# Optimization experiments

Hardware: AMD Instinct MI355X
Metric: run time of the kernel (lower is better)

## Reference

```python
import jax, jax.numpy as jnp
import numpy as np

ALPHA = 0.2  # LeakyReLU negative slope
NEG_INF = -9e15


def _xavier(key, shape, gain=1.414):
    fan_in, fan_out = shape[-2], shape[-1]
    lim = gain * np.sqrt(6.0 / (fan_in + fan_out))
    return jax.random.uniform(key, shape, jnp.float32, -lim, lim)


def setup_inputs() -> dict:
    key = jax.random.key(0)
    ks = jax.random.split(key, 8)
    B, N, Din, H, Dh, Do = 8, 1024, 256, 4, 128, 64
    x = jax.random.normal(ks[0], (B, N, Din), jnp.float32)
    adj = jax.random.randint(ks[1], (B, N, N), 0, 2).astype(jnp.int32)
    W_heads = _xavier(ks[2], (H, Din, Dh))                 # per-head W
    a_heads = _xavier(ks[3], (H, 2 * Dh, 1))[..., 0]       # per-head a, [H, 2*Dh]
    W_out = _xavier(ks[4], (H * Dh, Do))                   # out_att W
    a_out = _xavier(ks[5], (2 * Do, 1))[..., 0]            # out_att a, [2*Do]
    Wf = _xavier(ks[6], (Do, Do), gain=1.0)                # fc_out linear
    bf = jnp.zeros((Do,), jnp.float32)
    return {"x": x, "adj": adj, "W_heads": W_heads, "a_heads": a_heads,
            "W_out": W_out, "a_out": a_out, "Wf": Wf, "bf": bf}


def _leaky_relu(v):
    return jnp.where(v >= 0, v, ALPHA * v)


def _gat(h, adj, W, a):
    # h: [B,N,Fin], adj: [B,N,N], W: [Fin,Fout], a: [2*Fout]
    Wh = h @ W                                   # [B,N,F]
    F = W.shape[-1]
    # additive attention: e_ij = leakyrelu(a_src.Wh_i + a_dst.Wh_j)
    src = Wh @ a[:F]                             # [B,N]
    dst = Wh @ a[F:]                             # [B,N]
    e = _leaky_relu(src[:, :, None] + dst[:, None, :])   # [B,N,N]
    scores = jnp.where(adj > 0, e, NEG_INF)
    attn = jax.nn.softmax(scores, axis=-1)       # dropout is a no-op in eval
    return attn @ Wh                             # [B,N,F]


def reference(x, adj, W_heads, a_heads, W_out, a_out, Wf, bf):
    B, N, _ = x.shape
    H, _, Dh = W_heads.shape
    # multi-head GAT, heads vmapped over leading axis of W_heads / a_heads
    heads = jax.vmap(_gat, in_axes=(None, None, 0, 0))(x, adj, W_heads, a_heads)  # [H,B,N,Dh]
    xcat = jnp.moveaxis(heads, 0, 2).reshape(B, N, H * Dh)   # concat heads, dim=2
    out = jax.nn.elu(_gat(xcat, adj, W_out, a_out))           # [B,N,Do]
    out = jax.nn.relu(out @ Wf + bf)                          # fc_out (dropout no-op)
    return out
```

## Files before the change

### kernel.cpp

```cpp
#include <hip/hip_runtime.h>
#include <hip/hip_bf16.h>

#define BSZ 8
#define NN 1024
#define DIN 256
#define NH 4
#define DH 128
#define DOUT 64
#define RTOT (BSZ*NN)
#define FCAT (NH*DH)
#define ALPHA 0.2f
#define XBLK 1024

typedef unsigned short ushortT;
typedef __attribute__((ext_vector_type(8))) short bf16x8;
typedef __attribute__((ext_vector_type(4))) float f32x4;

static __device__ __forceinline__ ushortT f2bf(float f) {
    __hip_bfloat16 h = __float2bfloat16(f);
    return *reinterpret_cast<ushortT*>(&h);
}
static __device__ __forceinline__ float bfu2f(ushortT u) {
    return __uint_as_float(((unsigned)u) << 16);
}
static __device__ __forceinline__ void split2(float v, ushortT& hi, ushortT& lo) {
    hi = f2bf(v);
    lo = f2bf(v - bfu2f(hi));
}
static __device__ __forceinline__ void gload16(const ushortT* g, ushortT* l) {
    __builtin_amdgcn_global_load_lds(
        (const __attribute__((address_space(1))) unsigned int*)(const void*)g,
        (__attribute__((address_space(3))) unsigned int*)(void*)l, 16, 0, 0);
}

__global__ __launch_bounds__(256) void k_prepw(const float* __restrict__ x,
                                               const float* __restrict__ W,
                                               const float* __restrict__ Wout,
                                               ushortT* __restrict__ xbh, ushortT* __restrict__ xbl,
                                               ushortT* __restrict__ WbTh, ushortT* __restrict__ WbTl,
                                               ushortT* __restrict__ WoTh, ushortT* __restrict__ WoTl) {
    const int bx = blockIdx.x;
    if (bx < XBLK) {
        const int g = bx * 256 + threadIdx.x;
        const float4* p = (const float4*)x + (size_t)g * 2;
        union { ushortT u[8]; uint4 q; } th, tl;
#pragma unroll
        for (int e4 = 0; e4 < 2; ++e4) {
            const float4 v = p[e4];
            split2(v.x, th.u[e4 * 4 + 0], tl.u[e4 * 4 + 0]);
            split2(v.y, th.u[e4 * 4 + 1], tl.u[e4 * 4 + 1]);
            split2(v.z, th.u[e4 * 4 + 2], tl.u[e4 * 4 + 2]);
            split2(v.w, th.u[e4 * 4 + 3], tl.u[e4 * 4 + 3]);
        }
        ((uint4*)xbh)[g] = th.q;
        ((uint4*)xbl)[g] = tl.q;
        return;
    }
    const int g2 = (bx - XBLK) * 256 + threadIdx.x;
    if (g2 < NH * DH * DIN) {
        const int h = g2 >> 15, f = (g2 >> 8) & 127, k = g2 & 255;
        const int kt = k >> 6, k64 = k & 63;
        const float v = W[(size_t)h * DIN * DH + (size_t)k * DH + f];
        ushortT hi, lo; split2(v, hi, lo);
        const int idx = ((h * 4 + kt) * 128 + f) * 64 + k64;
        WbTh[idx] = hi; WbTl[idx] = lo;
    } else {
        const int g3 = g2 - NH * DH * DIN;
        const int f = g3 >> 9, k = g3 & 511;
        const float v = Wout[(size_t)k * DOUT + f];
        ushortT hi, lo; split2(v, hi, lo);
        WoTh[g3] = hi; WoTl[g3] = lo;
    }
}

__global__ __launch_bounds__(512) void k_main(const ushortT* __restrict__ xbh,
                                              const ushortT* __restrict__ xbl,
                                              const float* __restrict__ ah_,
                                              const ushortT* __restrict__ WbTh,
                                              const ushortT* __restrict__ WbTl,
                                              const int* __restrict__ adj,
                                              unsigned* __restrict__ adjbit,
                                              ushortT* __restrict__ WhT,
                                              float* __restrict__ src1,
                                              float* __restrict__ dst1) {
    __shared__ ushortT Ah[128 * 64], Al[128 * 64];
    __shared__ ushortT Bh[128 * 64], Bl[128 * 64];
    __shared__ float sred[8][32], dred[8][32];
    const int tid = threadIdx.x;
    if (blockIdx.x >= 256) {
        const int g = (blockIdx.x - 256) * 512 + tid;
        const int row = g >> 5, w = g & 31;
        const int4* p = (const int4*)(adj + (size_t)row * NN + w * 32);
        unsigned m = 0;
#pragma unroll
        for (int q = 0; q < 8; ++q) {
            const int4 v = p[q];
            m |= (v.x > 0 ? 1u : 0u) << (q * 4 + 0);
            m |= (v.y > 0 ? 1u : 0u) << (q * 4 + 1);
            m |= (v.z > 0 ? 1u : 0u) << (q * 4 + 2);
            m |= (v.w > 0 ? 1u : 0u) << (q * 4 + 3);
        }
        adjbit[g] = m;
        return;
    }
    const int lane = tid & 63, wave = tid >> 6;
    const int h = blockIdx.x >> 6, mt = blockIdx.x & 63;
    const int r0 = mt * 128, b = r0 >> 10, jr = r0 & 1023;
    const int m16 = lane & 15, quad = lane >> 4;
    const int mg = wave >> 1, fg = wave & 1;
    f32x4 acc[2][4];
#pragma unroll
    for (int a = 0; a < 2; ++a)
#pragma unroll
        for (int c = 0; c < 4; ++c) acc[a][c] = (f32x4){0.f, 0.f, 0.f, 0.f};

    for (int kt = 0; kt < 4; ++kt) {
        __syncthreads();
        const ushortT* planeH = WbTh + (size_t)((h * 4 + kt) * 128) * 64;
        const ushortT* planeL = WbTl + (size_t)((h * 4 + kt) * 128) * 64;
#pragma unroll
        for (int half = 0; half < 2; ++half) {
            const int f = wave * 16 + half * 8 + (lane >> 3);
            const int sc = (lane & 7) ^ (f & 7);
            gload16(planeH + (size_t)f * 64 + sc * 8, Bh + (wave * 16 + half * 8) * 64);
            gload16(planeL + (size_t)f * 64 + sc * 8, Bl + (wave * 16 + half * 8) * 64);
        }
#pragma unroll
        for (int half = 0; half < 2; ++half) {
            const int r = wave * 16 + half * 8 + (lane >> 3);
            const int sc = (lane & 7) ^ (r & 7);
            gload16(xbh + (size_t)(r0 + r) * DIN + kt * 64 + sc * 8, Ah + (wave * 16 + half * 8) * 64);
            gload16(xbl + (size_t)(r0 + r) * DIN + kt * 64 + sc * 8, Al + (wave * 16 + half * 8) * 64);
        }
        __syncthreads();
#pragma unroll
        for (int ks = 0; ks < 2; ++ks) {
            bf16x8 a_h[2], a_l[2], b_h[4], b_l[4];
#pragma unroll
            for (int ms = 0; ms < 2; ++ms) {
                const int row = (mg * 2 + ms) * 16 + m16;
                const int cl = (ks * 4 + quad) ^ (row & 7);
                a_h[ms] = *(const bf16x8*)&Ah[row * 64 + cl * 8];
                a_l[ms] = *(const bf16x8*)&Al[row * 64 + cl * 8];
            }
#pragma unroll
            for (int fs = 0; fs < 4; ++fs) {
                const int row = (fg * 4 + fs) * 16 + m16;
                const int cl = (ks * 4 + quad) ^ (row & 7);
                b_h[fs] = *(const bf16x8*)&Bh[row * 64 + cl * 8];
                b_l[fs] = *(const bf16x8*)&Bl[row * 64 + cl * 8];
            }
#pragma unroll
            for (int ms = 0; ms < 2; ++ms)
#pragma unroll
                for (int fs = 0; fs < 4; ++fs) {
                    acc[ms][fs] = __builtin_amdgcn_mfma_f32_16x16x32_bf16(a_h[ms], b_h[fs], acc[ms][fs], 0, 0, 0);
                    acc[ms][fs] = __builtin_amdgcn_mfma_f32_16x16x32_bf16(a_h[ms], b_l[fs], acc[ms][fs], 0, 0, 0);
                    acc[ms][fs] = __builtin_amdgcn_mfma_f32_16x16x32_bf16(a_l[ms], b_h[fs], acc[ms][fs], 0, 0, 0);
                }
        }
    }
    float sacc[2][4] = {{0,0,0,0},{0,0,0,0}}, dacc[2][4] = {{0,0,0,0},{0,0,0,0}};
#pragma unroll
    for (int ms = 0; ms < 2; ++ms)
#pragma unroll
        for (int fs = 0; fs < 4; ++fs) {
            const int fl = (fg * 4 + fs) * 16 + m16;
            const float a_s = ah_[h * 2 * DH + fl];
            const float a_d = ah_[h * 2 * DH + DH + fl];
            union { ushortT u[4]; uint2 q; } tw;
#pragma unroll
            for (int reg = 0; reg < 4; ++reg) {
                const float v = acc[ms][fs][reg];
                sacc[ms][reg] += v * a_s;
                dacc[ms][reg] += v * a_d;
                tw.u[reg] = f2bf(v);
            }
            *(uint2*)(WhT + ((size_t)((b * NH + h) * DH + fl)) * NN + jr + (mg * 2 + ms) * 16 + quad * 4) = tw.q;
        }
#pragma unroll
    for (int ms = 0; ms < 2; ++ms) {
#pragma unroll
        for (int reg = 0; reg < 4; ++reg) {
            float s = sacc[ms][reg], d = dacc[ms][reg];
#pragma unroll
            for (int o = 8; o > 0; o >>= 1) {
                s += __shfl_xor(s, o, 64);
                d += __shfl_xor(d, o, 64);
            }
            if (m16 == 0) {
                sred[wave][ms * 16 + quad * 4 + reg] = s;
                dred[wave][ms * 16 + quad * 4 + reg] = d;
            }
        }
    }
    __syncthreads();
    if (tid < 128) {
        const int mgr = tid >> 5, idx = tid & 31;
        src1[h * RTOT + r0 + tid] = sred[mgr * 2][idx] + sred[mgr * 2 + 1][idx];
        dst1[h * RTOT + r0 + tid] = dred[mgr * 2][idx] + dred[mgr * 2 + 1][idx];
    }
}

__global__ __launch_bounds__(512) void k_attn1(const unsigned* __restrict__ adjbit,
                                               const ushortT* __restrict__ WhT,
                                               const float* __restrict__ src1,
                                               const float* __restrict__ dst1,
                                               ushortT* __restrict__ xcat) {
    __shared__ ushortT As[2][64 * 64];
    __shared__ ushortT Bs[2][128 * 64];
    __shared__ unsigned maskS[64 * 32];
    __shared__ float dstv[NN];
    __shared__ float srcv[64], rowinv[64], red8[8];
    const int tid = threadIdx.x, lane = tid & 63, wave = tid >> 6;
    const int bh = blockIdx.x & 31, it = blockIdx.x >> 5;
    const int b = bh >> 2, h = bh & 3;
    const int i0 = it * 64;
    const int m16 = lane & 15, quad = lane >> 4;
    const int mg = wave >> 2, fg = wave & 3;

    const unsigned* mbase = adjbit + (size_t)(b * NN + i0) * 32;
#pragma unroll
    for (int k2 = 0; k2 < 4; ++k2) maskS[tid + 512 * k2] = mbase[tid + 512 * k2];
    float lm = -INFINITY;
#pragma unroll
    for (int k2 = 0; k2 < 2; ++k2) {
        const float d = dst1[h * RTOT + b * NN + tid + 512 * k2];
        dstv[tid + 512 * k2] = d;
        lm = fmaxf(lm, d);
    }
    if (tid < 64) srcv[tid] = src1[h * RTOT + b * NN + i0 + tid];
#pragma unroll
    for (int o = 32; o > 0; o >>= 1) lm = fmaxf(lm, __shfl_xor(lm, o, 64));
    if (lane == 0) red8[wave] = lm;
    __syncthreads();
    float dmax = red8[0];
#pragma unroll
    for (int w = 1; w < 8; ++w) dmax = fmaxf(dmax, red8[w]);

    const int arow = tid >> 3, apart = tid & 7;
    const float si = srcv[arow];
    float mrow = si + dmax;
    mrow = mrow >= 0.f ? mrow : ALPHA * mrow;
    float fsum = 0.f;

    const ushortT* Bbase = WhT + (size_t)(bh * DH) * NN;
    f32x4 acc[2][2];
#pragma unroll
    for (int a = 0; a < 2; ++a)
#pragma unroll
        for (int c = 0; c < 2; ++c) acc[a][c] = (f32x4){0.f, 0.f, 0.f, 0.f};

#define STAGE_TILE(kt_, buf_)                                                              \
    {                                                                                      \
        const int kt__ = (kt_);                                                            \
        ushortT* bdst = &Bs[(buf_)][0];                                                    \
        _Pragma("unroll")                                                                  \
        for (int half = 0; half < 2; ++half) {                                             \
            const int f = wave * 16 + half * 8 + (lane >> 3);                              \
            gload16(Bbase + (size_t)f * NN + kt__ * 64 + (((lane & 7) ^ (f & 7)) * 8),     \
                    bdst + (wave * 16 + half * 8) * 64);                                   \
        }                                                                                  \
        const unsigned w0 = maskS[arow * 32 + kt__ * 2 + (apart >> 2)];                    \
        const int bb = (apart & 3) * 8;                                                    \
        union { ushortT u[8]; uint4 q; } tw;                                               \
        _Pragma("unroll")                                                                  \
        for (int e4 = 0; e4 < 2; ++e4) {                                                   \
            const float4 dv = *(const float4*)&dstv[kt__ * 64 + apart * 8 + e4 * 4];       \
            const float vv[4] = {dv.x, dv.y, dv.z, dv.w};                                  \
            _Pragma("unroll")                                                              \
            for (int e = 0; e < 4; ++e) {                                                  \
                float v = si + vv[e];                                                      \
                v = v >= 0.f ? v : ALPHA * v;                                              \
                const unsigned bit = (w0 >> (bb + e4 * 4 + e)) & 1u;                       \
                const float p = bit ? __expf(v - mrow) : 0.f;                              \
                fsum += p;                                                                 \
                tw.u[e4 * 4 + e] = f2bf(p);                                                \
            }                                                                              \
        }                                                                                  \
        *(uint4*)&As[(buf_)][arow * 64 + (apart ^ (arow & 7)) * 8] = tw.q;                 \
    }

    STAGE_TILE(0, 0);
    for (int kt = 0; kt < 16; ++kt) {
        const int cb = kt & 1;
        __syncthreads();
        if (kt < 15) STAGE_TILE(kt + 1, cb ^ 1);
#pragma unroll
        for (int ks = 0; ks < 2; ++ks) {
            bf16x8 afr[2];
#pragma unroll
            for (int ms = 0; ms < 2; ++ms) {
                const int rowa = mg * 32 + ms * 16 + m16;
                const int cla = (ks * 4 + quad) ^ (rowa & 7);
                afr[ms] = *(const bf16x8*)&As[cb][rowa * 64 + cla * 8];
            }
#pragma unroll
            for (int ff = 0; ff < 2; ++ff) {
                const int rowb = fg * 32 + ff * 16 + m16;
                const int clb = (ks * 4 + quad) ^ (rowb & 7);
                const bf16x8 bfr = *(const bf16x8*)&Bs[cb][rowb * 64 + clb * 8];
#pragma unroll
                for (int ms = 0; ms < 2; ++ms)
                    acc[ms][ff] = __builtin_amdgcn_mfma_f32_16x16x32_bf16(afr[ms], bfr, acc[ms][ff], 0, 0, 0);
            }
        }
    }
#undef STAGE_TILE
#pragma unroll
    for (int o = 1; o < 8; o <<= 1) fsum += __shfl_xor(fsum, o, 64);
    if ((lane & 7) == 0) rowinv[arow] = 1.f / fsum;
    __syncthreads();
#pragma unroll
    for (int ms = 0; ms < 2; ++ms) {
        float rv[4];
#pragma unroll
        for (int reg = 0; reg < 4; ++reg) rv[reg] = rowinv[mg * 32 + ms * 16 + quad * 4 + reg];
#pragma unroll
        for (int ff = 0; ff < 2; ++ff) {
            const int f = h * DH + fg * 32 + ff * 16 + m16;
#pragma unroll
            for (int reg = 0; reg < 4; ++reg) {
                const int i = i0 + mg * 32 + ms * 16 + quad * 4 + reg;
                xcat[(size_t)(b * NN + i) * FCAT + f] = f2bf(acc[ms][ff][reg] * rv[reg]);
            }
        }
    }
}

__global__ __launch_bounds__(256) void k_wh2(const ushortT* __restrict__ xcat,
                                             const ushortT* __restrict__ WoTh,
                                             const ushortT* __restrict__ WoTl,
                                             const float* __restrict__ aout,
                                             ushortT* __restrict__ Wh2T,
                                             float* __restrict__ src2,
                                             float* __restrict__ dst2) {
    __shared__ ushortT As[32 * 64];
    __shared__ ushortT Bh[64 * 64], Bl[64 * 64];
    __shared__ float sred[4][16], dred[4][16];
    const int tid = threadIdx.x, lane = tid & 63, wave = tid >> 6;
    const int r0 = blockIdx.x * 32;
    const int b = r0 >> 10, jr = r0 & 1023;
    const int m16 = lane & 15, quad = lane >> 4;
    const int mg = wave >> 1, fg = wave & 1;
    f32x4 acc[2] = {(f32x4){0.f,0.f,0.f,0.f}, (f32x4){0.f,0.f,0.f,0.f}};

    for (int kt = 0; kt < 8; ++kt) {
        __syncthreads();
        {
            const int row = wave * 8 + (lane >> 3);
            const int sc = (lane & 7) ^ (row & 7);
            gload16(xcat + (size_t)(r0 + row) * FCAT + kt * 64 + sc * 8, As + wave * 8 * 64);
        }
#pragma unroll
        for (int half = 0; half < 2; ++half) {
            const int f = wave * 16 + half * 8 + (lane >> 3);
            const int sc = (lane & 7) ^ (f & 7);
            gload16(WoTh + (size_t)f * FCAT + kt * 64 + sc * 8, Bh + (wave * 16 + half * 8) * 64);
            gload16(WoTl + (size_t)f * FCAT + kt * 64 + sc * 8, Bl + (wave * 16 + half * 8) * 64);
        }
        __syncthreads();
#pragma unroll
        for (int ks = 0; ks < 2; ++ks) {
            const int rowa = mg * 16 + m16;
            const int cla = (ks * 4 + quad) ^ (rowa & 7);
            const bf16x8 afr = *(const bf16x8*)&As[rowa * 64 + cla * 8];
#pragma unroll
            for (int ff = 0; ff < 2; ++ff) {
                const int rowb = fg * 32 + ff * 16 + m16;
                const int clb = (ks * 4 + quad) ^ (rowb & 7);
                const bf16x8 b_h = *(const bf16x8*)&Bh[rowb * 64 + clb * 8];
                const bf16x8 b_l = *(const bf16x8*)&Bl[rowb * 64 + clb * 8];
                acc[ff] = __builtin_amdgcn_mfma_f32_16x16x32_bf16(afr, b_h, acc[ff], 0, 0, 0);
                acc[ff] = __builtin_amdgcn_mfma_f32_16x16x32_bf16(afr, b_l, acc[ff], 0, 0, 0);
            }
        }
    }
    float sv[4] = {0, 0, 0, 0}, dv[4] = {0, 0, 0, 0};
#pragma unroll
    for (int ff = 0; ff < 2; ++ff) {
        const int f = fg * 32 + ff * 16 + m16;
        const float a_s = aout[f], a_d = aout[DOUT + f];
        union { ushortT u[4]; uint2 q; } tw;
#pragma unroll
        for (int reg = 0; reg < 4; ++reg) {
            const float v = acc[ff][reg];
            sv[reg] += v * a_s;
            dv[reg] += v * a_d;
            tw.u[reg] = f2bf(v);
        }
        *(uint2*)(Wh2T + ((size_t)(b * DOUT + f)) * NN + jr + mg * 16 + quad * 4) = tw.q;
    }
#pragma unroll
    for (int reg = 0; reg < 4; ++reg) {
#pragma unroll
        for (int o = 8; o > 0; o >>= 1) {
            sv[reg] += __shfl_xor(sv[reg], o, 64);
            dv[reg] += __shfl_xor(dv[reg], o, 64);
        }
        if (m16 == 0) { sred[wave][quad * 4 + reg] = sv[reg]; dred[wave][quad * 4 + reg] = dv[reg]; }
    }
    __syncthreads();
    if (tid < 32) {
        const int mgr = tid >> 4, idx = tid & 15;
        src2[r0 + tid] = sred[mgr * 2][idx] + sred[mgr * 2 + 1][idx];
        dst2[r0 + tid] = dred[mgr * 2][idx] + dred[mgr * 2 + 1][idx];
    }
}

__global__ __launch_bounds__(256) void k_attn2(const unsigned* __restrict__ adjbit,
                                               const ushortT* __restrict__ Wh2T,
                                               const float* __restrict__ src2,
                                               const float* __restrict__ dst2,
                                               const float* __restrict__ Wf,
                                               const float* __restrict__ bfv,
                                               float* __restrict__ out) {
    __shared__ ushortT As[2][32 * 64];
    __shared__ ushortT Bs[2][64 * 64];
    __shared__ unsigned maskS[32 * 32];
    __shared__ float dstv[NN];
    __shared__ ushortT Wfh[64 * 64], Wfl[64 * 64];
    __shared__ float t2s[32 * 68];
    __shared__ float srcv[32], rowinv[32], red4[4];
    const int tid = threadIdx.x, lane = tid & 63, wave = tid >> 6;
    const int b = blockIdx.x & 7, it = blockIdx.x >> 3;
    const int i0 = it * 32;
    const int m16 = lane & 15, quad = lane >> 4;

    const unsigned* mbase = adjbit + (size_t)(b * NN + i0) * 32;
#pragma unroll
    for (int k2 = 0; k2 < 4; ++k2) maskS[tid + 256 * k2] = mbase[tid + 256 * k2];
    float lm = -INFINITY;
#pragma unroll
    for (int k2 = 0; k2 < 4; ++k2) {
        const float d = dst2[b * NN + tid + 256 * k2];
        dstv[tid + 256 * k2] = d;
        lm = fmaxf(lm, d);
    }
    if (tid < 32) srcv[tid] = src2[b * NN + i0 + tid];
    {
        const int c = tid & 63, kc = (tid >> 6) * 16;
        union { ushortT u[16]; uint4 q[2]; } th, tl;
#pragma unroll
        for (int e = 0; e < 16; ++e)
            split2(Wf[(size_t)(kc + e) * DOUT + c], th.u[e], tl.u[e]);
        const int s0 = ((tid >> 6) * 2) ^ (c & 7), s1 = ((tid >> 6) * 2 + 1) ^ (c & 7);
        *(uint4*)&Wfh[c * 64 + s0 * 8] = th.q[0];
        *(uint4*)&Wfh[c * 64 + s1 * 8] = th.q[1];
        *(uint4*)&Wfl[c * 64 + s0 * 8] = tl.q[0];
        *(uint4*)&Wfl[c * 64 + s1 * 8] = tl.q[1];
    }
#pragma unroll
    for (int o = 32; o > 0; o >>= 1) lm = fmaxf(lm, __shfl_xor(lm, o, 64));
    if (lane == 0) red4[wave] = lm;
    __syncthreads();
    const float dmax = fmaxf(fmaxf(red4[0], red4[1]), fmaxf(red4[2], red4[3]));

    const int arow = tid >> 3, apart = tid & 7;
    const float si = srcv[arow];
    float mrow = si + dmax;
    mrow = mrow >= 0.f ? mrow : ALPHA * mrow;
    float fsum = 0.f;

    const int mfrag = wave >> 1, fh = wave & 1;
    const ushortT* Bbase = Wh2T + (size_t)(b * DOUT) * NN;
    f32x4 acc[2] = {(f32x4){0.f,0.f,0.f,0.f}, (f32x4){0.f,0.f,0.f,0.f}};

#define STAGE2(kt_, buf_)                                                                  \
    {                                                                                      \
        const int kt__ = (kt_);                                                            \
        ushortT* bdst = &Bs[(buf_)][0];                                                    \
        _Pragma("unroll")                                                                  \
        for (int half = 0; half < 2; ++half) {                                             \
            const int f = wave * 16 + half * 8 + (lane >> 3);                              \
            gload16(Bbase + (size_t)f * NN + kt__ * 64 + (((lane & 7) ^ (f & 7)) * 8),     \
                    bdst + (wave * 16 + half * 8) * 64);                                   \
        }                                                                                  \
        const unsigned w0 = maskS[arow * 32 + kt__ * 2 + (apart >> 2)];                    \
        const int bb = (apart & 3) * 8;                                                    \
        union { ushortT u[8]; uint4 q; } tw;                                               \
        _Pragma("unroll")                                                                  \
        for (int e4 = 0; e4 < 2; ++e4) {                                                   \
            const float4 dv = *(const float4*)&dstv[kt__ * 64 + apart * 8 + e4 * 4];       \
            const float vv[4] = {dv.x, dv.y, dv.z, dv.w};                                  \
            _Pragma("unroll")                                                              \
            for (int e = 0; e < 4; ++e) {                                                  \
                float v = si + vv[e];                                                      \
                v = v >= 0.f ? v : ALPHA * v;                                              \
                const unsigned bit = (w0 >> (bb + e4 * 4 + e)) & 1u;                       \
                const float p = bit ? __expf(v - mrow) : 0.f;                              \
                fsum += p;                                                                 \
                tw.u[e4 * 4 + e] = f2bf(p);                                                \
            }                                                                              \
        }                                                                                  \
        *(uint4*)&As[(buf_)][arow * 64 + (apart ^ (arow & 7)) * 8] = tw.q;                 \
    }

    STAGE2(0, 0);
    for (int kt = 0; kt < 16; ++kt) {
        const int cb = kt & 1;
        __syncthreads();
        if (kt < 15) STAGE2(kt + 1, cb ^ 1);
#pragma unroll
        for (int ks = 0; ks < 2; ++ks) {
            const int rowa = mfrag * 16 + m16;
            const int cla = (ks * 4 + quad) ^ (rowa & 7);
            const bf16x8 afr = *(const bf16x8*)&As[cb][rowa * 64 + cla * 8];
#pragma unroll
            for (int ff = 0; ff < 2; ++ff) {
                const int rowb = (fh * 2 + ff) * 16 + m16;
                const int clb = (ks * 4 + quad) ^ (rowb & 7);
                const bf16x8 bfr = *(const bf16x8*)&Bs[cb][rowb * 64 + clb * 8];
                acc[ff] = __builtin_amdgcn_mfma_f32_16x16x32_bf16(afr, bfr, acc[ff], 0, 0, 0);
            }
        }
    }
#undef STAGE2
#pragma unroll
    for (int o = 1; o < 8; o <<= 1) fsum += __shfl_xor(fsum, o, 64);
    if ((lane & 7) == 0) rowinv[arow] = 1.f / fsum;
    __syncthreads();
#pragma unroll
    for (int ff = 0; ff < 2; ++ff) {
#pragma unroll
        for (int reg = 0; reg < 4; ++reg) {
            const int row = mfrag * 16 + quad * 4 + reg;
            float v = acc[ff][reg] * rowinv[row];
            v = v > 0.f ? v : (__expf(v) - 1.f);
            t2s[row * 68 + (fh * 2 + ff) * 16 + m16] = v;
        }
    }
    __syncthreads();
    const int mf = wave >> 1, nh = wave & 1;
    f32x4 oacc[2];
#pragma unroll
    for (int g = 0; g < 2; ++g) {
        const float bias = bfv[(nh * 2 + g) * 16 + m16];
        oacc[g] = (f32x4){bias, bias, bias, bias};
    }
#pragma unroll
    for (int ks = 0; ks < 2; ++ks) {
        const int rowa = mf * 16 + m16;
        const float4 fA = *(const float4*)&t2s[rowa * 68 + ks * 32 + quad * 8];
        const float4 fB = *(const float4*)&t2s[rowa * 68 + ks * 32 + quad * 8 + 4];
        union { ushortT u[8]; bf16x8 v; } a_h, a_l;
        const float av[8] = {fA.x, fA.y, fA.z, fA.w, fB.x, fB.y, fB.z, fB.w};
#pragma unroll
        for (int e = 0; e < 8; ++e) split2(av[e], a_h.u[e], a_l.u[e]);
#pragma unroll
        for (int g = 0; g < 2; ++g) {
            const int rowc = (nh * 2 + g) * 16 + m16;
            const int cl = (ks * 4 + quad) ^ (rowc & 7);
            const bf16x8 b_h = *(const bf16x8*)&Wfh[rowc * 64 + cl * 8];
            const bf16x8 b_l = *(const bf16x8*)&Wfl[rowc * 64 + cl * 8];
            oacc[g] = __builtin_amdgcn_mfma_f32_16x16x32_bf16(a_h.v, b_h, oacc[g], 0, 0, 0);
            oacc[g] = __builtin_amdgcn_mfma_f32_16x16x32_bf16(a_h.v, b_l, oacc[g], 0, 0, 0);
            oacc[g] = __builtin_amdgcn_mfma_f32_16x16x32_bf16(a_l.v, b_h, oacc[g], 0, 0, 0);
        }
    }
#pragma unroll
    for (int g = 0; g < 2; ++g) {
        const int c = (nh * 2 + g) * 16 + m16;
#pragma unroll
        for (int reg = 0; reg < 4; ++reg) {
            const int i = i0 + mf * 16 + quad * 4 + reg;
            out[(size_t)(b * NN + i) * DOUT + c] = fmaxf(oacc[g][reg], 0.f);
        }
    }
}

extern "C" void kernel_launch(void* const* d_in, const int* in_sizes, int n_in,
                              void* d_out, int out_size, void* d_ws, size_t ws_size,
                              hipStream_t stream) {
    const float* x   = (const float*)d_in[0];
    const int*   adj = (const int*)d_in[1];
    const float* Wh  = (const float*)d_in[2];
    const float* ah  = (const float*)d_in[3];
    const float* Wo  = (const float*)d_in[4];
    const float* ao  = (const float*)d_in[5];
    const float* Wf  = (const float*)d_in[6];
    const float* bf  = (const float*)d_in[7];
    float* out = (float*)d_out;

    float* ws    = (float*)d_ws;
    float* src1  = ws;
    float* dst1  = src1 + NH * RTOT;
    float* src2  = dst1 + NH * RTOT;
    float* dst2  = src2 + RTOT;
    ushortT* WhT   = (ushortT*)(dst2 + RTOT);
    ushortT* Wh2T  = WhT + (size_t)RTOT * FCAT;
    ushortT* xcat  = Wh2T + (size_t)RTOT * DOUT;
    ushortT* WbTh  = xcat + (size_t)RTOT * FCAT;
    ushortT* WbTl  = WbTh + NH * DH * DIN;
    ushortT* WoTh  = WbTl + NH * DH * DIN;
    ushortT* WoTl  = WoTh + DOUT * FCAT;
    unsigned* adjbit = (unsigned*)(WoTl + DOUT * FCAT);
    ushortT* xbh  = (ushortT*)(adjbit + (size_t)BSZ * NN * 32);
    ushortT* xbl  = xbh + (size_t)RTOT * DIN;

    hipLaunchKernelGGL(k_prepw, dim3(XBLK + (NH * DH * DIN + DOUT * FCAT) / 256), dim3(256), 0, stream,
                       x, Wh, Wo, xbh, xbl, WbTh, WbTl, WoTh, WoTl);
    hipLaunchKernelGGL(k_main,  dim3(768), dim3(512), 0, stream,
                       xbh, xbl, ah, WbTh, WbTl, adj, adjbit, WhT, src1, dst1);
    hipLaunchKernelGGL(k_attn1, dim3(512), dim3(512), 0, stream,
                       adjbit, WhT, src1, dst1, xcat);
    hipLaunchKernelGGL(k_wh2,   dim3(256), dim3(256), 0, stream,
                       xcat, WoTh, WoTl, ao, Wh2T, src2, dst2);
    hipLaunchKernelGGL(k_attn2, dim3(256), dim3(256), 0, stream,
                       adjbit, Wh2T, src2, dst2, Wf, bf, out);
}
```

Before: 154.1 us.

## Fuse all GAT stages into one cooperative persistent kernel with grid syncs

```diff
diff --git a/kernel.cpp b/kernel.cpp
--- a/kernel.cpp
+++ b/kernel.cpp
@@ -1,5 +1,8 @@
 #include <hip/hip_runtime.h>
 #include <hip/hip_bf16.h>
+#include <hip/hip_cooperative_groups.h>
+
+namespace cg = cooperative_groups;
 
 #define BSZ 8
 #define NN 1024
@@ -10,7 +13,6 @@
 #define RTOT (BSZ*NN)
 #define FCAT (NH*DH)
 #define ALPHA 0.2f
-#define XBLK 1024
 
 typedef unsigned short ushortT;
 typedef __attribute__((ext_vector_type(8))) short bf16x8;
@@ -33,538 +35,522 @@
         (__attribute__((address_space(3))) unsigned int*)(void*)l, 16, 0, 0);
 }
 
-__global__ __launch_bounds__(256) void k_prepw(const float* __restrict__ x,
-                                               const float* __restrict__ W,
-                                               const float* __restrict__ Wout,
-                                               ushortT* __restrict__ xbh, ushortT* __restrict__ xbl,
-                                               ushortT* __restrict__ WbTh, ushortT* __restrict__ WbTl,
-                                               ushortT* __restrict__ WoTh, ushortT* __restrict__ WoTl) {
+__global__ __launch_bounds__(512, 2) void k_mega(
+        const float* __restrict__ x, const int* __restrict__ adj,
+        const float* __restrict__ W, const float* __restrict__ ah_,
+        const float* __restrict__ Wout, const float* __restrict__ aout,
+        const float* __restrict__ Wf, const float* __restrict__ bfv,
+        float* __restrict__ out,
+        ushortT* __restrict__ xbh, ushortT* __restrict__ xbl,
+        ushortT* __restrict__ WbTh, ushortT* __restrict__ WbTl,
+        ushortT* __restrict__ WoTh, ushortT* __restrict__ WoTl,
+        unsigned* __restrict__ adjbit,
+        ushortT* __restrict__ WhT, float* __restrict__ src1, float* __restrict__ dst1,
+        ushortT* __restrict__ xcat, ushortT* __restrict__ Wh2T,
+        float* __restrict__ src2, float* __restrict__ dst2) {
+    __shared__ __align__(16) char smem[87424];
+    const int tid = threadIdx.x, lane = tid & 63, wave = tid >> 6;
     const int bx = blockIdx.x;
-    if (bx < XBLK) {
-        const int g = bx * 256 + threadIdx.x;
-        const float4* p = (const float4*)x + (size_t)g * 2;
-        union { ushortT u[8]; uint4 q; } th, tl;
-#pragma unroll
-        for (int e4 = 0; e4 < 2; ++e4) {
-            const float4 v = p[e4];
-            split2(v.x, th.u[e4 * 4 + 0], tl.u[e4 * 4 + 0]);
-            split2(v.y, th.u[e4 * 4 + 1], tl.u[e4 * 4 + 1]);
-            split2(v.z, th.u[e4 * 4 + 2], tl.u[e4 * 4 + 2]);
-            split2(v.w, th.u[e4 * 4 + 3], tl.u[e4 * 4 + 3]);
-        }
-        ((uint4*)xbh)[g] = th.q;
-        ((uint4*)xbl)[g] = tl.q;
-        return;
+    const int m16 = lane & 15, quad = lane >> 4;
+    cg::grid_group grid = cg::this_grid();
+
+    {
+        const int gth = bx * 512 + tid;
+#pragma unroll
+        for (int r = 0; r < 2; ++r) {
+            const int g = r * 131072 + gth;
+            const float4* p = (const float4*)x + (size_t)g * 2;
+            union { ushortT u[8]; uint4 q; } th, tl;
+#pragma unroll
+            for (int e4 = 0; e4 < 2; ++e4) {
+                const float4 v = p[e4];
+                split2(v.x, th.u[e4 * 4 + 0], tl.u[e4 * 4 + 0]);
+                split2(v.y, th.u[e4 * 4 + 1], tl.u[e4 * 4 + 1]);
+                split2(v.z, th.u[e4 * 4 + 2], tl.u[e4 * 4 + 2]);
+                split2(v.w, th.u[e4 * 4 + 3], tl.u[e4 * 4 + 3]);
+            }
+            ((uint4*)xbh)[g] = th.q;
+            ((uint4*)xbl)[g] = tl.q;
+        }
+        {
+            const int h = gth >> 15, f = (gth >> 8) & 127, k = gth & 255;
+            const int kt = k >> 6, k64 = k & 63;
+            const float v = W[(size_t)h * DIN * DH + (size_t)k * DH + f];
+            ushortT hi, lo; split2(v, hi, lo);
+            const int idx = ((h * 4 + kt) * 128 + f) * 64 + k64;
+            WbTh[idx] = hi; WbTl[idx] = lo;
+        }
+        if (gth < DOUT * FCAT) {
+            const int f = gth >> 9, k = gth & 511;
+            const float v = Wout[(size_t)k * DOUT + f];
+            ushortT hi, lo; split2(v, hi, lo);
+            WoTh[gth] = hi; WoTl[gth] = lo;
+        }
+#pragma unroll
+        for (int r = 0; r < 2; ++r) {
+            const int gw = r * 131072 + gth;
+            const int row = gw >> 5, w = gw & 31;
+            const int4* p = (const int4*)(adj + (size_t)row * NN + w * 32);
+            unsigned m = 0;
+#pragma unroll
+            for (int q = 0; q < 8; ++q) {
+                const int4 v = p[q];
+                m |= (v.x > 0 ? 1u : 0u) << (q * 4 + 0);
+                m |= (v.y > 0 ? 1u : 0u) << (q * 4 + 1);
+                m |= (v.z > 0 ? 1u : 0u) << (q * 4 + 2);
+                m |= (v.w > 0 ? 1u : 0u) << (q * 4 + 3);
+            }
+            adjbit[gw] = m;
+        }
     }
-    const int g2 = (bx - XBLK) * 256 + threadIdx.x;
-    if (g2 < NH * DH * DIN) {
-        const int h = g2 >> 15, f = (g2 >> 8) & 127, k = g2 & 255;
-        const int kt = k >> 6, k64 = k & 63;
-        const float v = W[(size_t)h * DIN * DH + (size_t)k * DH + f];
-        ushortT hi, lo; split2(v, hi, lo);
-        const int idx = ((h * 4 + kt) * 128 + f) * 64 + k64;
-        WbTh[idx] = hi; WbTl[idx] = lo;
-    } else {
-        const int g3 = g2 - NH * DH * DIN;
-        const int f = g3 >> 9, k = g3 & 511;
-        const float v = Wout[(size_t)k * DOUT + f];
-        ushortT hi, lo; split2(v, hi, lo);
-        WoTh[g3] = hi; WoTl[g3] = lo;
+    grid.sync();
+
+    {
+        ushortT* Ah = (ushortT*)smem;
+        ushortT* Al = Ah + 128 * 64;
+        ushortT* Bh = Al + 128 * 64;
+        ushortT* Bl = Bh + 128 * 64;
+        float* sred = (float*)(smem + 65536);
+        float* dred = sred + 256;
+        const int h = bx >> 6, mt = bx & 63;
+        const int r0 = mt * 128, b = r0 >> 10, jr = r0 & 1023;
+        const int mg = wave >> 1, fg = wave & 1;
+        f32x4 acc[2][4];
+#pragma unroll
+        for (int a = 0; a < 2; ++a)
+#pragma unroll
+            for (int c = 0; c < 4; ++c) acc[a][c] = (f32x4){0.f, 0.f, 0.f, 0.f};
+
+        for (int kt = 0; kt < 4; ++kt) {
+            __syncthreads();
+            const ushortT* planeH = WbTh + (size_t)((h * 4 + kt) * 128) * 64;
+            const ushortT* planeL = WbTl + (size_t)((h * 4 + kt) * 128) * 64;
+#pragma unroll
+            for (int half = 0; half < 2; ++half) {
+                const int f = wave * 16 + half * 8 + (lane >> 3);
+                const int sc = (lane & 7) ^ (f & 7);
+                gload16(planeH + (size_t)f * 64 + sc * 8, Bh + (wave * 16 + half * 8) * 64);
+                gload16(planeL + (size_t)f * 64 + sc * 8, Bl + (wave * 16 + half * 8) * 64);
+            }
+#pragma unroll
+            for (int half = 0; half < 2; ++half) {
+                const int r = wave * 16 + half * 8 + (lane >> 3);
+                const int sc = (lane & 7) ^ (r & 7);
+                gload16(xbh + (size_t)(r0 + r) * DIN + kt * 64 + sc * 8, Ah + (wave * 16 + half * 8) * 64);
+                gload16(xbl + (size_t)(r0 + r) * DIN + kt * 64 + sc * 8, Al + (wave * 16 + half * 8) * 64);
+            }
+            __syncthreads();
+#pragma unroll
+            for (int ks = 0; ks < 2; ++ks) {
+                bf16x8 a_h[2], a_l[2], b_h[4], b_l[4];
+#pragma unroll
+                for (int ms = 0; ms < 2; ++ms) {
+                    const int row = (mg * 2 + ms) * 16 + m16;
+                    const int cl = (ks * 4 + quad) ^ (row & 7);
+                    a_h[ms] = *(const bf16x8*)&Ah[row * 64 + cl * 8];
+                    a_l[ms] = *(const bf16x8*)&Al[row * 64 + cl * 8];
+                }
+#pragma unroll
+                for (int fs = 0; fs < 4; ++fs) {
+                    const int row = (fg * 4 + fs) * 16 + m16;
+                    const int cl = (ks * 4 + quad) ^ (row & 7);
+                    b_h[fs] = *(const bf16x8*)&Bh[row * 64 + cl * 8];
+                    b_l[fs] = *(const bf16x8*)&Bl[row * 64 + cl * 8];
+                }
+#pragma unroll
+                for (int ms = 0; ms < 2; ++ms)
+#pragma unroll
+                    for (int fs = 0; fs < 4; ++fs) {
+                        acc[ms][fs] = __builtin_amdgcn_mfma_f32_16x16x32_bf16(a_h[ms], b_h[fs], acc[ms][fs], 0, 0, 0);
+                        acc[ms][fs] = __builtin_amdgcn_mfma_f32_16x16x32_bf16(a_h[ms], b_l[fs], acc[ms][fs], 0, 0, 0);
+                        acc[ms][fs] = __builtin_amdgcn_mfma_f32_16x16x32_bf16(a_l[ms], b_h[fs], acc[ms][fs], 0, 0, 0);
+                    }
+            }
+        }
+        float sacc[2][4] = {{0,0,0,0},{0,0,0,0}}, dacc[2][4] = {{0,0,0,0},{0,0,0,0}};
+#pragma unroll
+        for (int ms = 0; ms < 2; ++ms)
+#pragma unroll
+            for (int fs = 0; fs < 4; ++fs) {
+                const int fl = (fg * 4 + fs) * 16 + m16;
+                const float a_s = ah_[h * 2 * DH + fl];
+                const float a_d = ah_[h * 2 * DH + DH + fl];
+                union { ushortT u[4]; uint2 q; } tw;
+#pragma unroll
+                for (int reg = 0; reg < 4; ++reg) {
+                    const float v = acc[ms][fs][reg];
+                    sacc[ms][reg] += v * a_s;
+                    dacc[ms][reg] += v * a_d;
+                    tw.u[reg] = f2bf(v);
+                }
+                *(uint2*)(WhT + ((size_t)((b * NH + h) * DH + fl)) * NN + jr + (mg * 2 + ms) * 16 + quad * 4) = tw.q;
+            }
+#pragma unroll
+        for (int ms = 0; ms < 2; ++ms) {
+#pragma unroll
+            for (int reg = 0; reg < 4; ++reg) {
+                float s = sacc[ms][reg], d = dacc[ms][reg];
+#pragma unroll
+                for (int o = 8; o > 0; o >>= 1) {
+                    s += __shfl_xor(s, o, 64);
+                    d += __shfl_xor(d, o, 64);
+                }
+                if (m16 == 0) {
+                    sred[wave * 32 + ms * 16 + quad * 4 + reg] = s;
+                    dred[wave * 32 + ms * 16 + quad * 4 + reg] = d;
+                }
+            }
+        }
+        __syncthreads();
+        if (tid < 128) {
+            const int mgr = tid >> 5, idx = tid & 31;
+            src1[h * RTOT + r0 + tid] = sred[mgr * 2 * 32 + idx] + sred[(mgr * 2 + 1) * 32 + idx];
+            dst1[h * RTOT + r0 + tid] = dred[mgr * 2 * 32 + idx] + dred[(mgr * 2 + 1) * 32 + idx];
+        }
     }
-}
-
-__global__ __launch_bounds__(512) void k_main(const ushortT* __restrict__ xbh,
-                                              const ushortT* __restrict__ xbl,
-                                              const float* __restrict__ ah_,
-                                              const ushortT* __restrict__ WbTh,
-                                              const ushortT* __restrict__ WbTl,
-                                              const int* __restrict__ adj,
-                                              unsigned* __restrict__ adjbit,
-                                              ushortT* __restrict__ WhT,
-                                              float* __restrict__ src1,
-                                              float* __restrict__ dst1) {
-    __shared__ ushortT Ah[128 * 64], Al[128 * 64];
-    __shared__ ushortT Bh[128 * 64], Bl[128 * 64];
-    __shared__ float sred[8][32], dred[8][32];
-    const int tid = threadIdx.x;
-    if (blockIdx.x >= 256) {
-        const int g = (blockIdx.x - 256) * 512 + tid;
-        const int row = g >> 5, w = g & 31;
-        const int4* p = (const int4*)(adj + (size_t)row * NN + w * 32);
-        unsigned m = 0;
-#pragma unroll
-        for (int q = 0; q < 8; ++q) {
-            const int4 v = p[q];
-            m |= (v.x > 0 ? 1u : 0u) << (q * 4 + 0);
-            m |= (v.y > 0 ? 1u : 0u) << (q * 4 + 1);
-            m |= (v.z > 0 ? 1u : 0u) << (q * 4 + 2);
-            m |= (v.w > 0 ? 1u : 0u) << (q * 4 + 3);
-        }
-        adjbit[g] = m;
-        return;
+    grid.sync();
+
+    {
+        ushortT* As2 = (ushortT*)smem;
+        ushortT* Bs2 = As2 + 2 * 128 * 64;
+        unsigned* mask2 = (unsigned*)(smem + 65536);
+        float* dstv2 = (float*)(smem + 65536 + 16384);
+        float* srcv2 = dstv2 + 1024;
+        float* rowinv2 = srcv2 + 128;
+        float* red8 = rowinv2 + 128;
+        const int bh = bx & 31, it = bx >> 5;
+        const int b = bh >> 2, h = bh & 3;
+        const int i0 = it * 128;
+
+        const unsigned* mbase = adjbit + (size_t)(b * NN + i0) * 32;
+#pragma unroll
+        for (int k2 = 0; k2 < 8; ++k2) mask2[tid + 512 * k2] = mbase[tid + 512 * k2];
+        float lm = -INFINITY;
+#pragma unroll
+        for (int k2 = 0; k2 < 2; ++k2) {
+            const float d = dst1[h * RTOT + b * NN + tid + 512 * k2];
+            dstv2[tid + 512 * k2] = d;
+            lm = fmaxf(lm, d);
+        }
+        if (tid < 128) srcv2[tid] = src1[h * RTOT + b * NN + i0 + tid];
+#pragma unroll
+        for (int o = 32; o > 0; o >>= 1) lm = fmaxf(lm, __shfl_xor(lm, o, 64));
+        if (lane == 0) red8[wave] = lm;
+        __syncthreads();
+        float dmax = red8[0];
+#pragma unroll
+        for (int w = 1; w < 8; ++w) dmax = fmaxf(dmax, red8[w]);
+
+        const int arow = tid >> 2, apart = tid & 3;
+        const float si = srcv2[arow];
+        float mrow = si + dmax;
+        mrow = mrow >= 0.f ? mrow : ALPHA * mrow;
+        float fsum = 0.f;
+
+        const ushortT* Bbase = WhT + (size_t)(bh * DH) * NN;
+        const int mg = wave >> 1, fg = wave & 1;
+        f32x4 acc[2][4];
+#pragma unroll
+        for (int a = 0; a < 2; ++a)
+#pragma unroll
+            for (int c = 0; c < 4; ++c) acc[a][c] = (f32x4){0.f, 0.f, 0.f, 0.f};
+
+#define STAGE2K(kt_, buf_)                                                                 \
+        {                                                                                  \
+            const int kt__ = (kt_);                                                        \
+            ushortT* bdst = Bs2 + (buf_) * 128 * 64;                                       \
+            _Pragma("unroll")                                                              \
+            for (int half = 0; half < 2; ++half) {                                         \
+                const int f = wave * 16 + half * 8 + (lane >> 3);                          \
+                gload16(Bbase + (size_t)f * NN + kt__ * 64 + (((lane & 7) ^ (f & 7)) * 8), \
+                        bdst + (wave * 16 + half * 8) * 64);                               \
+            }                                                                              \
+            const unsigned w0 = mask2[arow * 32 + kt__ * 2 + (apart >> 1)];                \
+            const int bb = (apart & 1) * 16;                                               \
+            union { ushortT u[16]; uint4 q[2]; } tw;                                       \
+            _Pragma("unroll")                                                              \
+            for (int e4 = 0; e4 < 4; ++e4) {                                               \
+                const float4 dv = *(const float4*)&dstv2[kt__ * 64 + apart * 16 + e4 * 4]; \
+                const float vv[4] = {dv.x, dv.y, dv.z, dv.w};                              \
+                _Pragma("unroll")                                                          \
+                for (int e = 0; e < 4; ++e) {                                              \
+                    float v = si + vv[e];                                                  \
+                    v = v >= 0.f ? v : ALPHA * v;                                          \
+                    const unsigned bit = (w0 >> (bb + e4 * 4 + e)) & 1u;                   \
+                    const float p = bit ? __expf(v - mrow) : 0.f;                          \
+                    fsum += p;                                                             \
+                    tw.u[e4 * 4 + e] = f2bf(p);                                            \
+                }                                                                          \
+            }                                                                              \
+            const int c0 = (apart * 2) ^ (arow & 7), c1 = (apart * 2 + 1) ^ (arow & 7);    \
+            ushortT* adst = As2 + (buf_) * 128 * 64 + arow * 64;                           \
+            *(uint4*)&adst[c0 * 8] = tw.q[0];                                              \
+            *(uint4*)&adst[c1 * 8] = tw.q[1];                                              \
+        }
+
+        STAGE2K(0, 0);
+        for (int kt = 0; kt < 16; ++kt) {
+            const int cb = kt & 1;
+            __syncthreads();
+            if (kt < 15) STAGE2K(kt + 1, cb ^ 1);
+            const ushortT* Asb = As2 + cb * 128 * 64;
+            const ushortT* Bsb = Bs2 + cb * 128 * 64;
+#pragma unroll
+            for (int ks = 0; ks < 2; ++ks) {
+                bf16x8 afr[2];
+#pragma unroll
+                for (int ms = 0; ms < 2; ++ms) {
+                    const int rowa = mg * 32 + ms * 16 + m16;
+                    const int cla = (ks * 4 + quad) ^ (rowa & 7);
+                    afr[ms] = *(const bf16x8*)&Asb[rowa * 64 + cla * 8];
+                }
+#pragma unroll
+                for (int ff = 0; ff < 4; ++ff) {
+                    const int rowb = fg * 64 + ff * 16 + m16;
+                    const int clb = (ks * 4 + quad) ^ (rowb & 7);
+                    const bf16x8 bfr = *(const bf16x8*)&Bsb[rowb * 64 + clb * 8];
+#pragma unroll
+                    for (int ms = 0; ms < 2; ++ms)
+                        acc[ms][ff] = __builtin_amdgcn_mfma_f32_16x16x32_bf16(afr[ms], bfr, acc[ms][ff], 0, 0, 0);
+                }
+            }
+        }
+#undef STAGE2K
+#pragma unroll
+        for (int o = 1; o < 4; o <<= 1) fsum += __shfl_xor(fsum, o, 64);
+        if ((lane & 3) == 0) rowinv2[arow] = 1.f / fsum;
+        __syncthreads();
+#pragma unroll
+        for (int ms = 0; ms < 2; ++ms) {
+            float rv[4];
+#pragma unroll
+            for (int reg = 0; reg < 4; ++reg) rv[reg] = rowinv2[mg * 32 + ms * 16 + quad * 4 + reg];
+#pragma unroll
+            for (int ff = 0; ff < 4; ++ff) {
+                const int f = h * DH + fg * 64 + ff * 16 + m16;
+#pragma unroll
+                for (int reg = 0; reg < 4; ++reg) {
+                    const int i = i0 + mg * 32 + ms * 16 + quad * 4 + reg;
+                    xcat[(size_t)(b * NN + i) * FCAT + f] = f2bf(acc[ms][ff][reg] * rv[reg]);
+                }
+            }
+        }
     }
-    const int lane = tid & 63, wave = tid >> 6;
-    const int h = blockIdx.x >> 6, mt = blockIdx.x & 63;
-    const int r0 = mt * 128, b = r0 >> 10, jr = r0 & 1023;
-    const int m16 = lane & 15, quad = lane >> 4;
-    const int mg = wave >> 1, fg = wave & 1;
-    f32x4 acc[2][4];
-#pragma unroll
-    for (int a = 0; a < 2; ++a)
-#pragma unroll
-        for (int c = 0; c < 4; ++c) acc[a][c] = (f32x4){0.f, 0.f, 0.f, 0.f};
-
-    for (int kt = 0; kt < 4; ++kt) {
-        __syncthreads();
-        const ushortT* planeH = WbTh + (size_t)((h * 4 + kt) * 128) * 64;
-        const ushortT* planeL = WbTl + (size_t)((h * 4 + kt) * 128) * 64;
-#pragma unroll
-        for (int half = 0; half < 2; ++half) {
-            const int f = wave * 16 + half * 8 + (lane >> 3);
-            const int sc = (lane & 7) ^ (f & 7);
-            gload16(planeH + (size_t)f * 64 + sc * 8, Bh + (wave * 16 + half * 8) * 64);
-            gload16(planeL + (size_t)f * 64 + sc * 8, Bl + (wave * 16 + half * 8) * 64);
-        }
-#pragma unroll
-        for (int half = 0; half < 2; ++half) {
-            const int r = wave * 16 + half * 8 + (lane >> 3);
-            const int sc = (lane & 7) ^ (r & 7);
-            gload16(xbh + (size_t)(r0 + r) * DIN + kt * 64 + sc * 8, Ah + (wave * 16 + half * 8) * 64);
-            gload16(xbl + (size_t)(r0 + r) * DIN + kt * 64 + sc * 8, Al + (wave * 16 + half * 8) * 64);
-        }
-        __syncthreads();
-#pragma unroll
-        for (int ks = 0; ks < 2; ++ks) {
-            bf16x8 a_h[2], a_l[2], b_h[4], b_l[4];
-#pragma unroll
-            for (int ms = 0; ms < 2; ++ms) {
-                const int row = (mg * 2 + ms) * 16 + m16;
-                const int cl = (ks * 4 + quad) ^ (row & 7);
-                a_h[ms] = *(const bf16x8*)&Ah[row * 64 + cl * 8];
-                a_l[ms] = *(const bf16x8*)&Al[row * 64 + cl * 8];
-            }
-#pragma unroll
-            for (int fs = 0; fs < 4; ++fs) {
-                const int row = (fg * 4 + fs) * 16 + m16;
-                const int cl = (ks * 4 + quad) ^ (row & 7);
-                b_h[fs] = *(const bf16x8*)&Bh[row * 64 + cl * 8];
-                b_l[fs] = *(const bf16x8*)&Bl[row * 64 + cl * 8];
-            }
-#pragma unroll
-            for (int ms = 0; ms < 2; ++ms)
-#pragma unroll
-                for (int fs = 0; fs < 4; ++fs) {
-                    acc[ms][fs] = __builtin_amdgcn_mfma_f32_16x16x32_bf16(a_h[ms], b_h[fs], acc[ms][fs], 0, 0, 0);
-                    acc[ms][fs] = __builtin_amdgcn_mfma_f32_16x16x32_bf16(a_h[ms], b_l[fs], acc[ms][fs], 0, 0, 0);
-                    acc[ms][fs] = __builtin_amdgcn_mfma_f32_16x16x32_bf16(a_l[ms], b_h[fs], acc[ms][fs], 0, 0, 0);
-                }
+    grid.sync();
+
+    {
+        ushortT* As3 = (ushortT*)smem;
+        ushortT* B3h = As3 + 8 * 32 * 64;
+        ushortT* B3l = B3h + 2 * 64 * 64;
+        float* sred3 = (float*)(smem + 65536);
+        float* dred3 = sred3 + 128;
+        const int r0 = bx * 32, b = r0 >> 10, jr = r0 & 1023;
+        const int mfrag = wave >> 2, fq = wave & 3;
+
+#pragma unroll
+        for (int half = 0; half < 4; ++half) {
+            const int row = half * 8 + (lane >> 3);
+            const int sc = (lane & 7) ^ (row & 7);
+            gload16(xcat + (size_t)(r0 + row) * FCAT + wave * 64 + sc * 8, As3 + wave * 2048 + half * 512);
+        }
+#define S3B(kt_, buf_)                                                                     \
+        {                                                                                  \
+            const int f = wave * 8 + (lane >> 3);                                          \
+            const int sc = (lane & 7) ^ (f & 7);                                           \
+            gload16(WoTh + (size_t)f * FCAT + (kt_) * 64 + sc * 8, B3h + (buf_) * 4096 + wave * 512); \
+            gload16(WoTl + (size_t)f * FCAT + (kt_) * 64 + sc * 8, B3l + (buf_) * 4096 + wave * 512); \
+        }
+        f32x4 acc3 = (f32x4){0.f, 0.f, 0.f, 0.f};
+        S3B(0, 0);
+        for (int kt = 0; kt < 8; ++kt) {
+            const int cb = kt & 1;
+            __syncthreads();
+            if (kt < 7) S3B(kt + 1, cb ^ 1);
+#pragma unroll
+            for (int ks = 0; ks < 2; ++ks) {
+                const int rowa = mfrag * 16 + m16;
+                const int cla = (ks * 4 + quad) ^ (rowa & 7);
+                const bf16x8 afr = *(const bf16x8*)&As3[kt * 2048 + rowa * 64 + cla * 8];
+                const int rowb = fq * 16 + m16;
+                const int clb = (ks * 4 + quad) ^ (rowb & 7);
+                const bf16x8 b_h = *(const bf16x8*)&B3h[cb * 4096 + rowb * 64 + clb * 8];
+                const bf16x8 b_l = *(const bf16x8*)&B3l[cb * 4096 + rowb * 64 + clb * 8];
+                acc3 = __builtin_amdgcn_mfma_f32_16x16x32_bf16(afr, b_h, acc3, 0, 0, 0);
+                acc3 = __builtin_amdgcn_mfma_f32_16x16x32_bf16(afr, b_l, acc3, 0, 0, 0);
+            }
+        }
+#undef S3B
+        {
+            const int f = fq * 16 + m16;
+            const float a_s = aout[f], a_d = aout[DOUT + f];
+            float sv[4], dv[4];
+            union { ushortT u[4]; uint2 q; } tw;
+#pragma unroll
+            for (int reg = 0; reg < 4; ++reg) {
+                const float v = acc3[reg];
+                sv[reg] = v * a_s;
+                dv[reg] = v * a_d;
+                tw.u[reg] = f2bf(v);
+            }
+            *(uint2*)(Wh2T + ((size_t)(b * DOUT + f)) * NN + jr + mfrag * 16 + quad * 4) = tw.q;
+#pragma unroll
+            for (int reg = 0; reg < 4; ++reg) {
+#pragma unroll
+                for (int o = 1; o < 16; o <<= 1) {
+                    sv[reg] += __shfl_xor(sv[reg], o, 64);
+                    dv[reg] += __shfl_xor(dv[reg], o, 64);
+                }
+                if (m16 == 0) {
+                    sred3[wave * 16 + quad * 4 + reg] = sv[reg];
+                    dred3[wave * 16 + quad * 4 + reg] = dv[reg];
+                }
+            }
+        }
+        __syncthreads();
+        if (tid < 32) {
+            const int mf = tid >> 4, idx = tid & 15;
+            float s = 0.f, d = 0.f;
+#pragma unroll
+            for (int q = 0; q < 4; ++q) {
+                s += sred3[(mf * 4 + q) * 16 + idx];
+                d += dred3[(mf * 4 + q) * 16 + idx];
+            }
+            src2[r0 + tid] = s;
+            dst2[r0 + tid] = d;
         }
     }
-    float sacc[2][4] = {{0,0,0,0},{0,0,0,0}}, dacc[2][4] = {{0,0,0,0},{0,0,0,0}};
-#pragma unroll
-    for (int ms = 0; ms < 2; ++ms)
-#pragma unroll
-        for (int fs = 0; fs < 4; ++fs) {
-            const int fl = (fg * 4 + fs) * 16 + m16;
-            const float a_s = ah_[h * 2 * DH + fl];
-            const float a_d = ah_[h * 2 * DH + DH + fl];
-            union { ushortT u[4]; uint2 q; } tw;
-#pragma unroll
-            for (int reg = 0; reg < 4; ++reg) {
-                const float v = acc[ms][fs][reg];
-                sacc[ms][reg] += v * a_s;
-                dacc[ms][reg] += v * a_d;
-                tw.u[reg] = f2bf(v);
-            }
-            *(uint2*)(WhT + ((size_t)((b * NH + h) * DH + fl)) * NN + jr + (mg * 2 + ms) * 16 + quad * 4) = tw.q;
-        }
-#pragma unroll
-    for (int ms = 0; ms < 2; ++ms) {
-#pragma unroll
-        for (int reg = 0; reg < 4; ++reg) {
-            float s = sacc[ms][reg], d = dacc[ms][reg];
-#pragma unroll
-            for (int o = 8; o > 0; o >>= 1) {
-                s += __shfl_xor(s, o, 64);
-                d += __shfl_xor(d, o, 64);
-            }
-            if (m16 == 0) {
-                sred[wave][ms * 16 + quad * 4 + reg] = s;
-                dred[wave][ms * 16 + quad * 4 + reg] = d;
-            }
-        }
-    }
-    __syncthreads();
-    if (tid < 128) {
-        const int mgr = tid >> 5, idx = tid & 31;
-        src1[h * RTOT + r0 + tid] = sred[mgr * 2][idx] + sred[mgr * 2 + 1][idx];
-        dst1[h * RTOT + r0 + tid] = dred[mgr * 2][idx] + dred[mgr * 2 + 1][idx];
-    }
-}
-
-__global__ __launch_bounds__(512) void k_attn1(const unsigned* __restrict__ adjbit,
-                                               const ushortT* __restrict__ WhT,
-                                               const float* __restrict__ src1,
-                                               const float* __restrict__ dst1,
-                                               ushortT* __restrict__ xcat) {
-    __shared__ ushortT As[2][64 * 64];
-    __shared__ ushortT Bs[2][128 * 64];
-    __shared__ unsigned maskS[64 * 32];
-    __shared__ float dstv[NN];
-    __shared__ float srcv[64], rowinv[64], red8[8];
-    const int tid = threadIdx.x, lane = tid & 63, wave = tid >> 6;
-    const int bh = blockIdx.x & 31, it = blockIdx.x >> 5;
-    const int b = bh >> 2, h = bh & 3;
-    const int i0 = it * 64;
-    const int m16 = lane & 15, quad = lane >> 4;
-    const int mg = wave >> 2, fg = wave & 3;
-
-    const unsigned* mbase = adjbit + (size_t)(b * NN + i0) * 32;
-#pragma unroll
-    for (int k2 = 0; k2 < 4; ++k2) maskS[tid + 512 * k2] = mbase[tid + 512 * k2];
-    float lm = -INFINITY;
-#pragma unroll
-    for (int k2 = 0; k2 < 2; ++k2) {
-        const float d = dst1[h * RTOT + b * NN + tid + 512 * k2];
-        dstv[tid + 512 * k2] = d;
-        lm = fmaxf(lm, d);
-    }
-    if (tid < 64) srcv[tid] = src1[h * RTOT + b * NN + i0 + tid];
-#pragma unroll
-    for (int o = 32; o > 0; o >>= 1) lm = fmaxf(lm, __shfl_xor(lm, o, 64));
-    if (lane == 0) red8[wave] = lm;
-    __syncthreads();
-    float dmax = red8[0];
-#pragma unroll
-    for (int w = 1; w < 8; ++w) dmax = fmaxf(dmax, red8[w]);
-
-    const int arow = tid >> 3, apart = tid & 7;
-    const float si = srcv[arow];
-    float mrow = si + dmax;
-    mrow = mrow >= 0.f ? mrow : ALPHA * mrow;
-    float fsum = 0.f;
-
-    const ushortT* Bbase = WhT + (size_t)(bh * DH) * NN;
-    f32x4 acc[2][2];
-#pragma unroll
-    for (int a = 0; a < 2; ++a)
-#pragma unroll
-        for (int c = 0; c < 2; ++c) acc[a][c] = (f32x4){0.f, 0.f, 0.f, 0.f};
-
-#define STAGE_TILE(kt_, buf_)                                                              \
-    {                                                                                      \
-        const int kt__ = (kt_);                                                            \
-        ushortT* bdst = &Bs[(buf_)][0];                                                    \
-        _Pragma("unroll")                                                                  \
-        for (int half = 0; half < 2; ++half) {                                             \
-            const int f = wave * 16 + half * 8 + (lane >> 3);                              \
+    grid.sync();
+
+    {
+        ushortT* As4 = (ushortT*)smem;
+        ushortT* Bs4 = As4 + 2 * 32 * 64;
+        ushortT* Wfh4 = Bs4 + 2 * 64 * 64;
+        ushortT* Wfl4 = Wfh4 + 64 * 64;
+        unsigned* mask4 = (unsigned*)(smem + 40960);
+        float* dstv4 = (float*)(smem + 45056);
+        float* t2s = (float*)(smem + 49152);
+        float* srcv4 = (float*)(smem + 57856);
+        float* rowinv4 = srcv4 + 32;
+        float* red8b = rowinv4 + 32;
+        const int b = bx & 7, it = bx >> 3, i0 = it * 32;
+
+        const unsigned* mbase = adjbit + (size_t)(b * NN + i0) * 32;
+#pragma unroll
+        for (int k2 = 0; k2 < 2; ++k2) mask4[tid + 512 * k2] = mbase[tid + 512 * k2];
+        float lm = -INFINITY;
+#pragma unroll
+        for (int k2 = 0; k2 < 2; ++k2) {
+            const float d = dst2[b * NN + tid + 512 * k2];
+            dstv4[tid + 512 * k2] = d;
+            lm = fmaxf(lm, d);
+        }
+        if (tid < 32) srcv4[tid] = src2[b * NN + i0 + tid];
+        {
+            const int c = tid & 63, kc = wave * 8;
+            union { ushortT u[8]; uint4 q; } th4, tl4;
+#pragma unroll
+            for (int e = 0; e < 8; ++e)
+                split2(Wf[(size_t)(kc + e) * DOUT + c], th4.u[e], tl4.u[e]);
+            const int ch = wave ^ (c & 7);
+            *(uint4*)&Wfh4[c * 64 + ch * 8] = th4.q;
+            *(uint4*)&Wfl4[c * 64 + ch * 8] = tl4.q;
+        }
+#pragma unroll
+        for (int o = 32; o > 0; o >>= 1) lm = fmaxf(lm, __shfl_xor(lm, o, 64));
+        if (lane == 0) red8b[wave] = lm;
+        __syncthreads();
+        float dmax = red8b[0];
+#pragma unroll
+        for (int w = 1; w < 8; ++w) dmax = fmaxf(dmax, red8b[w]);
+
+        const int arow = tid >> 4, apart = tid & 15;
+        const float si = srcv4[arow];
+        float mrow = si + dmax;
+        mrow = mrow >= 0.f ? mrow : ALPHA * mrow;
+        float fsum = 0.f;
+
+        const int mfrag = wave >> 2, fq = wave & 3;
+        const ushortT* Bbase = Wh2T + (size_t)(b * DOUT) * NN;
+        f32x4 acc4 = (f32x4){0.f, 0.f, 0.f, 0.f};
+
+#define STAGE4K(kt_, buf_)                                                                 \
+        {                                                                                  \
+            const int kt__ = (kt_);                                                        \
+            const int f = wave * 8 + (lane >> 3);                                          \
             gload16(Bbase + (size_t)f * NN + kt__ * 64 + (((lane & 7) ^ (f & 7)) * 8),     \
-                    bdst + (wave * 16 + half * 8) * 64);                                   \
-        }                                                                                  \
-        const unsigned w0 = maskS[arow * 32 + kt__ * 2 + (apart >> 2)];                    \
-        const int bb = (apart & 3) * 8;                                                    \
-        union { ushortT u[8]; uint4 q; } tw;                                               \
-        _Pragma("unroll")                                                                  \
-        for (int e4 = 0; e4 < 2; ++e4) {                                                   \
-            const float4 dv = *(const float4*)&dstv[kt__ * 64 + apart * 8 + e4 * 4];       \
+                    Bs4 + (buf_) * 4096 + wave * 512);                                     \
+            const unsigned w0 = mask4[arow * 32 + kt__ * 2 + (apart >> 3)];                \
+            const int bb = (apart & 7) * 4;                                                \
+            union { ushortT u[4]; uint2 q; } tw;                                           \
+            const float4 dv = *(const float4*)&dstv4[kt__ * 64 + apart * 4];               \
             const float vv[4] = {dv.x, dv.y, dv.z, dv.w};                                  \
             _Pragma("unroll")                                                              \
             for (int e = 0; e < 4; ++e) {                                                  \
                 float v = si + vv[e];                                                      \
                 v = v >= 0.f ? v : ALPHA * v;                                              \
-                const unsigned bit = (w0 >> (bb + e4 * 4 + e)) & 1u;                       \
+                const unsigned bit = (w0 >> (bb + e)) & 1u;                                \
                 const float p = bit ? __expf(v - mrow) : 0.f;                              \
                 fsum += p;                                                                 \
-                tw.u[e4 * 4 + e] = f2bf(p);                                                \
+                tw.u[e] = f2bf(p);                                                         \
             }                                                                              \
-        }                                                                                  \
-        *(uint4*)&As[(buf_)][arow * 64 + (apart ^ (arow & 7)) * 8] = tw.q;                 \
-    }
-
-    STAGE_TILE(0, 0);
-    for (int kt = 0; kt < 16; ++kt) {
-        const int cb = kt & 1;
-        __syncthreads();
-        if (kt < 15) STAGE_TILE(kt + 1, cb ^ 1);
-#pragma unroll
-        for (int ks = 0; ks < 2; ++ks) {
-            bf16x8 afr[2];
-#pragma unroll
-            for (int ms = 0; ms < 2; ++ms) {
-                const int rowa = mg * 32 + ms * 16 + m16;
+            *(uint2*)&As4[(buf_) * 2048 + arow * 64 + (((apart >> 1) ^ (arow & 7)) * 8) + (apart & 1) * 4] = tw.q; \
+        }
+
+        STAGE4K(0, 0);
+        for (int kt = 0; kt < 16; ++kt) {
+            const int cb = kt & 1;
+            __syncthreads();
+            if (kt < 15) STAGE4K(kt + 1, cb ^ 1);
+#pragma unroll
+            for (int ks = 0; ks < 2; ++ks) {
+                const int rowa = mfrag * 16 + m16;
                 const int cla = (ks * 4 + quad) ^ (rowa & 7);
-                afr[ms] = *(const bf16x8*)&As[cb][rowa * 64 + cla * 8];
-            }
-#pragma unroll
-            for (int ff = 0; ff < 2; ++ff) {
-                const int rowb = fg * 32 + ff * 16 + m16;
+                const bf16x8 afr = *(const bf16x8*)&As4[cb * 2048 + rowa * 64 + cla * 8];
+                const int rowb = fq * 16 + m16;
                 const int clb = (ks * 4 + quad) ^ (rowb & 7);
-                const bf16x8 bfr = *(const bf16x8*)&Bs[cb][rowb * 64 + clb * 8];
-#pragma unroll
-                for (int ms = 0; ms < 2; ++ms)
-                    acc[ms][ff] = __builtin_amdgcn_mfma_f32_16x16x32_bf16(afr[ms], bfr, acc[ms][ff], 0, 0, 0);
-            }
-        }
-    }
-#undef STAGE_TILE
-#pragma unroll
-    for (int o = 1; o < 8; o <<= 1) fsum += __shfl_xor(fsum, o, 64);
-    if ((lane & 7) == 0) rowinv[arow] = 1.f / fsum;
-    __syncthreads();
-#pragma unroll
-    for (int ms = 0; ms < 2; ++ms) {
-        float rv[4];
-#pragma unroll
-        for (int reg = 0; reg < 4; ++reg) rv[reg] = rowinv[mg * 32 + ms * 16 + quad * 4 + reg];
-#pragma unroll
-        for (int ff = 0; ff < 2; ++ff) {
-            const int f = h * DH + fg * 32 + ff * 16 + m16;
-#pragma unroll
-            for (int reg = 0; reg < 4; ++reg) {
-                const int i = i0 + mg * 32 + ms * 16 + quad * 4 + reg;
-                xcat[(size_t)(b * NN + i) * FCAT + f] = f2bf(acc[ms][ff][reg] * rv[reg]);
-            }
-        }
-    }
-}
-
-__global__ __launch_bounds__(256) void k_wh2(const ushortT* __restrict__ xcat,
-                                             const ushortT* __restrict__ WoTh,
-                                             const ushortT* __restrict__ WoTl,
-                                             const float* __restrict__ aout,
-                                             ushortT* __restrict__ Wh2T,
-                                             float* __restrict__ src2,
-                                             float* __restrict__ dst2) {
-    __shared__ ushortT As[32 * 64];
-    __shared__ ushortT Bh[64 * 64], Bl[64 * 64];
-    __shared__ float sred[4][16], dred[4][16];
-    const int tid = threadIdx.x, lane = tid & 63, wave = tid >> 6;
-    const int r0 = blockIdx.x * 32;
-    const int b = r0 >> 10, jr = r0 & 1023;
-    const int m16 = lane & 15, quad = lane >> 4;
-    const int mg = wave >> 1, fg = wave & 1;
-    f32x4 acc[2] = {(f32x4){0.f,0.f,0.f,0.f}, (f32x4){0.f,0.f,0.f,0.f}};
-
-    for (int kt = 0; kt < 8; ++kt) {
-        __syncthreads();
+                const bf16x8 bfr = *(const bf16x8*)&Bs4[cb * 4096 + rowb * 64 + clb * 8];
+                acc4 = __builtin_amdgcn_mfma_f32_16x16x32_bf16(afr, bfr, acc4, 0, 0, 0);
+            }
+        }
+#undef STAGE4K
+#pragma unroll
+        for (int o = 1; o < 16; o <<= 1) fsum += __shfl_xor(fsum, o, 64);
+        if ((lane & 15) == 0) rowinv4[arow] = 1.f / fsum;
+        __syncthreads();
+#pragma unroll
+        for (int reg = 0; reg < 4; ++reg) {
+            const int row = mfrag * 16 + quad * 4 + reg;
+            float v = acc4[reg] * rowinv4[row];
+            v = v > 0.f ? v : (__expf(v) - 1.f);
+            t2s[row * 68 + fq * 16 + m16] = v;
+        }
+        __syncthreads();
+        const int cc = fq * 16 + m16;
+        f32x4 oacc;
         {
-            const int row = wave * 8 + (lane >> 3);
-            const int sc = (lane & 7) ^ (row & 7);
-            gload16(xcat + (size_t)(r0 + row) * FCAT + kt * 64 + sc * 8, As + wave * 8 * 64);
-        }
-#pragma unroll
-        for (int half = 0; half < 2; ++half) {
-            const int f = wave * 16 + half * 8 + (lane >> 3);
-            const int sc = (lane & 7) ^ (f & 7);
-            gload16(WoTh + (size_t)f * FCAT + kt * 64 + sc * 8, Bh + (wave * 16 + half * 8) * 64);
-            gload16(WoTl + (size_t)f * FCAT + kt * 64 + sc * 8, Bl + (wave * 16 + half * 8) * 64);
-        }
-        __syncthreads();
-#pragma unroll
-        for (int ks = 0; ks < 2; ++ks) {
-            const int rowa = mg * 16 + m16;
-            const int cla = (ks * 4 + quad) ^ (rowa & 7);
-            const bf16x8 afr = *(const bf16x8*)&As[rowa * 64 + cla * 8];
-#pragma unroll
-            for (int ff = 0; ff < 2; ++ff) {
-                const int rowb = fg * 32 + ff * 16 + m16;
-                const int clb = (ks * 4 + quad) ^ (rowb & 7);
-                const bf16x8 b_h = *(const bf16x8*)&Bh[rowb * 64 + clb * 8];
-                const bf16x8 b_l = *(const bf16x8*)&Bl[rowb * 64 + clb * 8];
-                acc[ff] = __builtin_amdgcn_mfma_f32_16x16x32_bf16(afr, b_h, acc[ff], 0, 0, 0);
-                acc[ff] = __builtin_amdgcn_mfma_f32_16x16x32_bf16(afr, b_l, acc[ff], 0, 0, 0);
-            }
-        }
-    }
-    float sv[4] = {0, 0, 0, 0}, dv[4] = {0, 0, 0, 0};
-#pragma unroll
-    for (int ff = 0; ff < 2; ++ff) {
-        const int f = fg * 32 + ff * 16 + m16;
-        const float a_s = aout[f], a_d = aout[DOUT + f];
-        union { ushortT u[4]; uint2 q; } tw;
-#pragma unroll
-        for (int reg = 0; reg < 4; ++reg) {
-            const float v = acc[ff][reg];
-            sv[reg] += v * a_s;
-            dv[reg] += v * a_d;
-            tw.u[reg] = f2bf(v);
-        }
-        *(uint2*)(Wh2T + ((size_t)(b * DOUT + f)) * NN + jr + mg * 16 + quad * 4) = tw.q;
-    }
-#pragma unroll
-    for (int reg = 0; reg < 4; ++reg) {
-#pragma unroll
-        for (int o = 8; o > 0; o >>= 1) {
-            sv[reg] += __shfl_xor(sv[reg], o, 64);
-            dv[reg] += __shfl_xor(dv[reg], o, 64);
-        }
-        if (m16 == 0) { sred[wave][quad * 4 + reg] = sv[reg]; dred[wave][quad * 4 + reg] = dv[reg]; }
-    }
-    __syncthreads();
-    if (tid < 32) {
-        const int mgr = tid >> 4, idx = tid & 15;
-        src2[r0 + tid] = sred[mgr * 2][idx] + sred[mgr * 2 + 1][idx];
-        dst2[r0 + tid] = dred[mgr * 2][idx] + dred[mgr * 2 + 1][idx];
-    }
-}
-
-__global__ __launch_bounds__(256) void k_attn2(const unsigned* __restrict__ adjbit,
-                                               const ushortT* __restrict__ Wh2T,
-                                               const float* __restrict__ src2,
-                                               const float* __restrict__ dst2,
-                                               const float* __restrict__ Wf,
-                                               const float* __restrict__ bfv,
-                                               float* __restrict__ out) {
-    __shared__ ushortT As[2][32 * 64];
-    __shared__ ushortT Bs[2][64 * 64];
-    __shared__ unsigned maskS[32 * 32];
-    __shared__ float dstv[NN];
-    __shared__ ushortT Wfh[64 * 64], Wfl[64 * 64];
-    __shared__ float t2s[32 * 68];
-    __shared__ float srcv[32], rowinv[32], red4[4];
-    const int tid = threadIdx.x, lane = tid & 63, wave = tid >> 6;
-    const int b = blockIdx.x & 7, it = blockIdx.x >> 3;
-    const int i0 = it * 32;
-    const int m16 = lane & 15, quad = lane >> 4;
-
-    const unsigned* mbase = adjbit + (size_t)(b * NN + i0) * 32;
-#pragma unroll
-    for (int k2 = 0; k2 < 4; ++k2) maskS[tid + 256 * k2] = mbase[tid + 256 * k2];
-    float lm = -INFINITY;
-#pragma unroll
-    for (int k2 = 0; k2 < 4; ++k2) {
-        const float d = dst2[b * NN + tid + 256 * k2];
-        dstv[tid + 256 * k2] = d;
-        lm = fmaxf(lm, d);
-    }
-    if (tid < 32) srcv[tid] = src2[b * NN + i0 + tid];
-    {
-        const int c = tid & 63, kc = (tid >> 6) * 16;
-        union { ushortT u[16]; uint4 q[2]; } th, tl;
-#pragma unroll
-        for (int e = 0; e < 16; ++e)
-            split2(Wf[(size_t)(kc + e) * DOUT + c], th.u[e], tl.u[e]);
-        const int s0 = ((tid >> 6) * 2) ^ (c & 7), s1 = ((tid >> 6) * 2 + 1) ^ (c & 7);
-        *(uint4*)&Wfh[c * 64 + s0 * 8] = th.q[0];
-        *(uint4*)&Wfh[c * 64 + s1 * 8] = th.q[1];
-        *(uint4*)&Wfl[c * 64 + s0 * 8] = tl.q[0];
-        *(uint4*)&Wfl[c * 64 + s1 * 8] = tl.q[1];
-    }
-#pragma unroll
-    for (int o = 32; o > 0; o >>= 1) lm = fmaxf(lm, __shfl_xor(lm, o, 64));
-    if (lane == 0) red4[wave] = lm;
-    __syncthreads();
-    const float dmax = fmaxf(fmaxf(red4[0], red4[1]), fmaxf(red4[2], red4[3]));
-
-    const int arow = tid >> 3, apart = tid & 7;
-    const float si = srcv[arow];
-    float mrow = si + dmax;
-    mrow = mrow >= 0.f ? mrow : ALPHA * mrow;
-    float fsum = 0.f;
-
-    const int mfrag = wave >> 1, fh = wave & 1;
-    const ushortT* Bbase = Wh2T + (size_t)(b * DOUT) * NN;
-    f32x4 acc[2] = {(f32x4){0.f,0.f,0.f,0.f}, (f32x4){0.f,0.f,0.f,0.f}};
-
-#define STAGE2(kt_, buf_)                                                                  \
-    {                                                                                      \
-        const int kt__ = (kt_);                                                            \
-        ushortT* bdst = &Bs[(buf_)][0];                                                    \
-        _Pragma("unroll")                                                                  \
-        for (int half = 0; half < 2; ++half) {                                             \
-            const int f = wave * 16 + half * 8 + (lane >> 3);                              \
-            gload16(Bbase + (size_t)f * NN + kt__ * 64 + (((lane & 7) ^ (f & 7)) * 8),     \
-                    bdst + (wave * 16 + half * 8) * 64);                                   \
-        }                                                                                  \
-        const unsigned w0 = maskS[arow * 32 + kt__ * 2 + (apart >> 2)];                    \
-        const int bb = (apart & 3) * 8;                                                    \
-        union { ushortT u[8]; uint4 q; } tw;                                               \
-        _Pragma("unroll")                                                                  \
-        for (int e4 = 0; e4 < 2; ++e4) {                                                   \
-            const float4 dv = *(const float4*)&dstv[kt__ * 64 + apart * 8 + e4 * 4];       \
-            const float vv[4] = {dv.x, dv.y, dv.z, dv.w};                                  \
-            _Pragma("unroll")                                                              \
-            for (int e = 0; e < 4; ++e) {                                                  \
-                float v = si + vv[e];                                                      \
-                v = v >= 0.f ? v : ALPHA * v;                                              \
-                const unsigned bit = (w0 >> (bb + e4 * 4 + e)) & 1u;                       \
-                const float p = bit ? __expf(v - mrow) : 0.f;                              \
-                fsum += p;                                                                 \
-                tw.u[e4 * 4 + e] = f2bf(p);                                                \
-            }                                                                              \
-        }                                                                                  \
-        *(uint4*)&As[(buf_)][arow * 64 + (apart ^ (arow & 7)) * 8] = tw.q;                 \
-    }
-
-    STAGE2(0, 0);
-    for (int kt = 0; kt < 16; ++kt) {
-        const int cb = kt & 1;
-        __syncthreads();
-        if (kt < 15) STAGE2(kt + 1, cb ^ 1);
+            const float bias = bfv[cc];
+            oacc = (f32x4){bias, bias, bias, bias};
+        }
 #pragma unroll
         for (int ks = 0; ks < 2; ++ks) {
             const int rowa = mfrag * 16 + m16;
-            const int cla = (ks * 4 + quad) ^ (rowa & 7);
-            const bf16x8 afr = *(const bf16x8*)&As[cb][rowa * 64 + cla * 8];
-#pragma unroll
-            for (int ff = 0; ff < 2; ++ff) {
-                const int rowb = (fh * 2 + ff) * 16 + m16;
-                const int clb = (ks * 4 + quad) ^ (rowb & 7);
-                const bf16x8 bfr = *(const bf16x8*)&Bs[cb][rowb * 64 + clb * 8];
-                acc[ff] = __builtin_amdgcn_mfma_f32_16x16x32_bf16(afr, bfr, acc[ff], 0, 0, 0);
-            }
-        }
-    }
-#undef STAGE2
-#pragma unroll
-    for (int o = 1; o < 8; o <<= 1) fsum += __shfl_xor(fsum, o, 64);
-    if ((lane & 7) == 0) rowinv[arow] = 1.f / fsum;
-    __syncthreads();
-#pragma unroll
-    for (int ff = 0; ff < 2; ++ff) {
+            const float4 fA = *(const float4*)&t2s[rowa * 68 + ks * 32 + quad * 8];
+            const float4 fB = *(const float4*)&t2s[rowa * 68 + ks * 32 + quad * 8 + 4];
+            union { ushortT u[8]; bf16x8 v; } a_h, a_l;
+            const float av[8] = {fA.x, fA.y, fA.z, fA.w, fB.x, fB.y, fB.z, fB.w};
+#pragma unroll
+            for (int e = 0; e < 8; ++e) split2(av[e], a_h.u[e], a_l.u[e]);
+            const int cl = (ks * 4 + quad) ^ (cc & 7);
+            const bf16x8 b_h = *(const bf16x8*)&Wfh4[cc * 64 + cl * 8];
+            const bf16x8 b_l = *(const bf16x8*)&Wfl4[cc * 64 + cl * 8];
+            oacc = __builtin_amdgcn_mfma_f32_16x16x32_bf16(a_h.v, b_h, oacc, 0, 0, 0);
+            oacc = __builtin_amdgcn_mfma_f32_16x16x32_bf16(a_h.v, b_l, oacc, 0, 0, 0);
+            oacc = __builtin_amdgcn_mfma_f32_16x16x32_bf16(a_l.v, b_h, oacc, 0, 0, 0);
+        }
 #pragma unroll
         for (int reg = 0; reg < 4; ++reg) {
-            const int row = mfrag * 16 + quad * 4 + reg;
-            float v = acc[ff][reg] * rowinv[row];
-            v = v > 0.f ? v : (__expf(v) - 1.f);
-            t2s[row * 68 + (fh * 2 + ff) * 16 + m16] = v;
-        }
-    }
-    __syncthreads();
-    const int mf = wave >> 1, nh = wave & 1;
-    f32x4 oacc[2];
-#pragma unroll
-    for (int g = 0; g < 2; ++g) {
-        const float bias = bfv[(nh * 2 + g) * 16 + m16];
-        oacc[g] = (f32x4){bias, bias, bias, bias};
-    }
-#pragma unroll
-    for (int ks = 0; ks < 2; ++ks) {
-        const int rowa = mf * 16 + m16;
-        const float4 fA = *(const float4*)&t2s[rowa * 68 + ks * 32 + quad * 8];
-        const float4 fB = *(const float4*)&t2s[rowa * 68 + ks * 32 + quad * 8 + 4];
-        union { ushortT u[8]; bf16x8 v; } a_h, a_l;
-        const float av[8] = {fA.x, fA.y, fA.z, fA.w, fB.x, fB.y, fB.z, fB.w};
-#pragma unroll
-        for (int e = 0; e < 8; ++e) split2(av[e], a_h.u[e], a_l.u[e]);
-#pragma unroll
-        for (int g = 0; g < 2; ++g) {
-            const int rowc = (nh * 2 + g) * 16 + m16;
-            const int cl = (ks * 4 + quad) ^ (rowc & 7);
-            const bf16x8 b_h = *(const bf16x8*)&Wfh[rowc * 64 + cl * 8];
-            const bf16x8 b_l = *(const bf16x8*)&Wfl[rowc * 64 + cl * 8];
-            oacc[g] = __builtin_amdgcn_mfma_f32_16x16x32_bf16(a_h.v, b_h, oacc[g], 0, 0, 0);
-            oacc[g] = __builtin_amdgcn_mfma_f32_16x16x32_bf16(a_h.v, b_l, oacc[g], 0, 0, 0);
-            oacc[g] = __builtin_amdgcn_mfma_f32_16x16x32_bf16(a_l.v, b_h, oacc[g], 0, 0, 0);
-        }
-    }
-#pragma unroll
-    for (int g = 0; g < 2; ++g) {
-        const int c = (nh * 2 + g) * 16 + m16;
-#pragma unroll
-        for (int reg = 0; reg < 4; ++reg) {
-            const int i = i0 + mf * 16 + quad * 4 + reg;
-            out[(size_t)(b * NN + i) * DOUT + c] = fmaxf(oacc[g][reg], 0.f);
+            const int i = i0 + mfrag * 16 + quad * 4 + reg;
+            out[(size_t)(b * NN + i) * DOUT + cc] = fmaxf(oacc[reg], 0.f);
         }
     }
 }
@@ -598,14 +584,13 @@
     ushortT* xbh  = (ushortT*)(adjbit + (size_t)BSZ * NN * 32);
     ushortT* xbl  = xbh + (size_t)RTOT * DIN;
 
-    hipLaunchKernelGGL(k_prepw, dim3(XBLK + (NH * DH * DIN + DOUT * FCAT) / 256), dim3(256), 0, stream,
-                       x, Wh, Wo, xbh, xbl, WbTh, WbTl, WoTh, WoTl);
-    hipLaunchKernelGGL(k_main,  dim3(768), dim3(512), 0, stream,
-                       xbh, xbl, ah, WbTh, WbTl, adj, adjbit, WhT, src1, dst1);
-    hipLaunchKernelGGL(k_attn1, dim3(512), dim3(512), 0, stream,
-                       adjbit, WhT, src1, dst1, xcat);
-    hipLaunchKernelGGL(k_wh2,   dim3(256), dim3(256), 0, stream,
-                       xcat, WoTh, WoTl, ao, Wh2T, src2, dst2);
-    hipLaunchKernelGGL(k_attn2, dim3(256), dim3(256), 0, stream,
-                       adjbit, Wh2T, src2, dst2, Wf, bf, out);
+    void* args[] = {
+        (void*)&x, (void*)&adj, (void*)&Wh, (void*)&ah, (void*)&Wo, (void*)&ao,
+        (void*)&Wf, (void*)&bf, (void*)&out,
+        (void*)&xbh, (void*)&xbl, (void*)&WbTh, (void*)&WbTl,
+        (void*)&WoTh, (void*)&WoTl, (void*)&adjbit,
+        (void*)&WhT, (void*)&src1, (void*)&dst1,
+        (void*)&xcat, (void*)&Wh2T, (void*)&src2, (void*)&dst2
+    };
+    hipLaunchCooperativeKernel((const void*)k_mega, dim3(256), dim3(512), args, 0, stream);
 }
```

Result: slower. 285.4 us (+85.2%).
